# Performance work log

Measured on AMD Instinct MI355X. Metric: run time of the kernel, lower is better.

Reference implementation:

```python
import jax, jax.numpy as jnp
import numpy as np

B, IN_UNITS, IN_CHANNELS, NUM_UNITS, UNIT_SIZE = 128, 32, 4096, 10, 16
NUM_ITER = 3


def setup_inputs() -> dict:
    key = jax.random.key(0)
    k1, k2 = jax.random.split(key)
    # x: primary-capsule output [B, in_units, in_channels]
    x = jax.random.normal(k1, (B, IN_UNITS, IN_CHANNELS), dtype=jnp.float32)
    # W: routing weights, torch param shape [1, C, J, D, K] with batch dim dropped
    W = jax.random.normal(k2, (IN_CHANNELS, NUM_UNITS, UNIT_SIZE, IN_UNITS), dtype=jnp.float32)
    return {"x": x, "W": W}


def reference(x, W):
    b_sz = x.shape[0]
    C, J = W.shape[0], W.shape[1]
    # torch: x.transpose(1,2) -> [B,C,K]; u_hat = W @ x -> [B,C,J,D,1]
    # u_hat[b,i,j,d] = sum_k W[i,j,d,k] * x[b,k,i]
    u_hat = jnp.einsum('ijdk,bki->bijd', W, x)  # [B, C, J, D]
    b_ij = jnp.zeros((C, J), dtype=x.dtype)
    v = None
    for _ in range(NUM_ITER):
        # faithful: softmax over dim=1 (in_channels axis), not over classes
        c_ij = jax.nn.softmax(b_ij, axis=0)               # [C, J]
        s = jnp.einsum('ij,bijd->bjd', c_ij, u_hat)        # [B, J, D]
        # faithful squash: original sums over dim=2 of [B,1,J,D,1] == class axis J
        mag_sq = jnp.sum(s * s, axis=1, keepdims=True)     # [B, 1, D]
        v = (mag_sq / (1.0 + mag_sq)) * (s / jnp.sqrt(mag_sq))
        # agreement: <u_hat, v> averaged over batch
        agree = jnp.einsum('bijd,bjd->ij', u_hat, v) / b_sz
        b_ij = b_ij + agree
    # torch returns v_j.squeeze(1): [B, J, D, 1]
    return v[:, :, :, None]
```

## Files before the change

kernel.cpp:

```cpp
#include <hip/hip_runtime.h>


typedef __attribute__((ext_vector_type(8))) __bf16 bf16x8;
typedef __attribute__((ext_vector_type(4))) float  f32x4;
typedef __attribute__((ext_vector_type(8))) unsigned short u16x8;
typedef __attribute__((ext_vector_type(4))) unsigned short u16x4;

#define DI __device__ __forceinline__

DI float bf2f(unsigned short u){ unsigned int x = ((unsigned int)u) << 16; return __builtin_bit_cast(float, x); }
DI unsigned short f2bf(float f){
  unsigned int u = __builtin_bit_cast(unsigned int, f);
  u += 0x7fffu + ((u >> 16) & 1u);
  return (unsigned short)(u >> 16);
}

constexpr int Ci = 4096, Kk = 32, Jj = 10, Dd = 16, Bb = 128;
constexpr int KI = Ci * Kk;
constexpr int JDt = Jj * Dd;
constexpr int NCH = 256, CK = 512;

constexpr size_t OFF_XB = 0;
constexpr size_t SZ_XB  = (size_t)Bb * KI * 2;
constexpr size_t OFF_W2 = OFF_XB + SZ_XB;
constexpr size_t SZ_W2  = (size_t)JDt * KI * 2;
constexpr size_t OFF_BT = OFF_W2 + SZ_W2;
constexpr size_t SZ_BT  = (size_t)Jj * Ci * 4;
constexpr size_t OFF_CT = OFF_BT + SZ_BT;
constexpr size_t OFF_VBT = OFF_CT + SZ_BT;
constexpr size_t SZ_VBT = (size_t)JDt * Bb * 2;
constexpr size_t OFF_SP = OFF_VBT + SZ_VBT;
constexpr size_t SZ_SP  = (size_t)NCH * Bb * JDt * 4;

__global__ __launch_bounds__(256) void pack_x(const float* __restrict__ x, unsigned short* __restrict__ xbf){
  const size_t e = (size_t)blockIdx.x * 256 + threadIdx.x;
  const float4* xv = (const float4*)x;
  float4 a = xv[e*2], b = xv[e*2+1];
  u16x8 o;
  o[0]=f2bf(a.x); o[1]=f2bf(a.y); o[2]=f2bf(a.z); o[3]=f2bf(a.w);
  o[4]=f2bf(b.x); o[5]=f2bf(b.y); o[6]=f2bf(b.z); o[7]=f2bf(b.w);
  *(u16x8*)(xbf + e*8) = o;
}

__global__ __launch_bounds__(256) void pack_w2(const float* __restrict__ W, unsigned short* __restrict__ w2){
  __shared__ float tile[64][65];
  const int mt = blockIdx.x % 80, it = blockIdx.x / 80;
  const int m0 = mt * 64, i0 = it * 64;
  #pragma unroll
  for(int u=0; u<4; u++){
    int e = threadIdx.x + 256*u;
    int il = e >> 4, q = e & 15;
    float4 v = *(const float4*)(W + (size_t)(i0+il)*5120 + m0 + q*4);
    tile[il][q*4+0]=v.x; tile[il][q*4+1]=v.y; tile[il][q*4+2]=v.z; tile[il][q*4+3]=v.w;
  }
  __syncthreads();
  #pragma unroll
  for(int u=0; u<4; u++){
    int e = threadIdx.x + 256*u;
    int ml = e >> 4, q = e & 15;
    u16x4 o;
    o[0]=f2bf(tile[q*4+0][ml]); o[1]=f2bf(tile[q*4+1][ml]);
    o[2]=f2bf(tile[q*4+2][ml]); o[3]=f2bf(tile[q*4+3][ml]);
    *(u16x4*)(w2 + (size_t)(m0+ml)*Ci + i0 + q*4) = o;
  }
}

__global__ __launch_bounds__(256) void softmax_k(const float* __restrict__ bT, float* __restrict__ cT){
  const int j = blockIdx.x, tid = threadIdx.x, lane = tid & 63, wid = tid >> 6;
  __shared__ float red[4];
  float vals[16];
  float mx = -3.4e38f;
  #pragma unroll
  for(int u=0; u<16; u++){ vals[u] = bT[j*Ci + tid + 256*u]; mx = fmaxf(mx, vals[u]); }
  #pragma unroll
  for(int o=32; o>0; o>>=1) mx = fmaxf(mx, __shfl_xor(mx, o));
  if(lane == 0) red[wid] = mx;
  __syncthreads();
  mx = fmaxf(fmaxf(red[0],red[1]), fmaxf(red[2],red[3]));
  float sm = 0.f;
  #pragma unroll
  for(int u=0; u<16; u++){ vals[u] = expf(vals[u]-mx); sm += vals[u]; }
  #pragma unroll
  for(int o=32; o>0; o>>=1) sm += __shfl_xor(sm, o);
  __syncthreads();
  if(lane == 0) red[wid] = sm;
  __syncthreads();
  sm = red[0]+red[1]+red[2]+red[3];
  float inv = 1.0f / sm;
  #pragma unroll
  for(int u=0; u<16; u++) cT[j*Ci + tid + 256*u] = vals[u]*inv;
}

__global__ __launch_bounds__(512) void s_pass(const unsigned short* __restrict__ xb,
                                              const unsigned short* __restrict__ w2,
                                              const float* __restrict__ cT,
                                              float* __restrict__ spart){
  __shared__ unsigned short xs[128*64];
  __shared__ unsigned short wsm[160*64];
  const int tid = threadIdx.x, lane = tid & 63, wid = tid >> 6;
  const int wb = wid & 3, wj = wid >> 2;
  const int ki0 = blockIdx.x * CK;
  f32x4 acc[2][5];
  const f32x4 z = {0.f,0.f,0.f,0.f};
  #pragma unroll
  for(int m=0;m<2;m++){ acc[m][0]=z; acc[m][1]=z; acc[m][2]=z; acc[m][3]=z; acc[m][4]=z; }

  for(int step=0; step<CK/64; ++step){
    const int kb = ki0 + step*64;
    const int ib = kb & (Ci-1);
    #pragma unroll
    for(int u=0; u<2; u++){
      int e = tid + 512*u;
      int b = e >> 3, sg = e & 7;
      u16x8 v = *(const u16x8*)(xb + (size_t)b*KI + kb + sg*8);
      *(u16x8*)((char*)xs + b*128 + ((sg*16) ^ ((b&7)<<4))) = v;
    }
    #pragma unroll
    for(int u=0; u<3; u++){
      int e = tid + 512*u;
      if(e < 1280){
        int jd = e >> 3, sg = e & 7;
        u16x8 v = *(const u16x8*)(w2 + (size_t)jd*KI + kb + sg*8);
        const float* cp = cT + (jd>>4)*Ci + ib + sg*8;
        float4 c0 = *(const float4*)cp;
        float4 c1 = *(const float4*)(cp+4);
        u16x8 o;
        o[0]=f2bf(bf2f(v[0])*c0.x); o[1]=f2bf(bf2f(v[1])*c0.y);
        o[2]=f2bf(bf2f(v[2])*c0.z); o[3]=f2bf(bf2f(v[3])*c0.w);
        o[4]=f2bf(bf2f(v[4])*c1.x); o[5]=f2bf(bf2f(v[5])*c1.y);
        o[6]=f2bf(bf2f(v[6])*c1.z); o[7]=f2bf(bf2f(v[7])*c1.w);
        *(u16x8*)((char*)wsm + jd*128 + ((sg*16) ^ ((jd&7)<<4))) = o;
      }
    }
    __syncthreads();
    #pragma unroll
    for(int ks=0; ks<2; ks++){
      const int kk2 = (ks*32 + ((lane>>4)<<3)) * 2;
      bf16x8 a[2];
      #pragma unroll
      for(int m=0;m<2;m++){
        int row = wb*32 + m*16 + (lane&15);
        a[m] = *(const bf16x8*)((const char*)xs + row*128 + (kk2 ^ ((row&7)<<4)));
      }
      #pragma unroll
      for(int n=0;n<5;n++){
        int row = wj*80 + n*16 + (lane&15);
        bf16x8 bb = *(const bf16x8*)((const char*)wsm + row*128 + (kk2 ^ ((row&7)<<4)));
        acc[0][n] = __builtin_amdgcn_mfma_f32_16x16x32_bf16(a[0], bb, acc[0][n], 0,0,0);
        acc[1][n] = __builtin_amdgcn_mfma_f32_16x16x32_bf16(a[1], bb, acc[1][n], 0,0,0);
      }
    }
    __syncthreads();
  }
  float* sp = spart + (size_t)blockIdx.x * (Bb*JDt);
  #pragma unroll
  for(int m=0;m<2;m++)
    #pragma unroll
    for(int n=0;n<5;n++)
      #pragma unroll
      for(int r=0;r<4;r++){
        int b  = wb*32 + m*16 + ((lane>>4)<<2) + r;
        int jd = wj*80 + n*16 + (lane&15);
        sp[b*JDt + jd] = acc[m][n][r];
      }
}

__global__ __launch_bounds__(256) void redsq(const float* __restrict__ spart,
                                             float* __restrict__ vout,
                                             unsigned short* __restrict__ vbT){
  const int b = blockIdx.x, tid = threadIdx.x;
  __shared__ float sq[JDt];
  __shared__ float scale[Dd];
  float s = 0.f;
  if(tid < JDt){
    const float* p = spart + b*JDt + tid;
    #pragma unroll 8
    for(int ch=0; ch<NCH; ch++) s += p[(size_t)ch*(Bb*JDt)];
    sq[tid] = s*s;
  }
  __syncthreads();
  if(tid < Dd){
    float m = 0.f;
    #pragma unroll
    for(int j=0;j<Jj;j++) m += sq[j*Dd + tid];
    scale[tid] = sqrtf(m) / (1.0f + m);
  }
  __syncthreads();
  if(tid < JDt){
    float v = s * scale[tid & (Dd-1)];
    vout[b*JDt + tid] = v;
    vbT[tid*Bb + b] = f2bf(v);
  }
}

__global__ __launch_bounds__(256) void agree_pass(const unsigned short* __restrict__ xb,
                                                  const unsigned short* __restrict__ vbT,
                                                  const unsigned short* __restrict__ w2,
                                                  float* __restrict__ bT){
  __shared__ unsigned short xsT[64*128];
  __shared__ unsigned short vsm[160*128];
  const int tid = threadIdx.x, lane = tid & 63, wid = tid >> 6;
  const int wj = wid & 1, wk = wid >> 1;
  const int ki0 = blockIdx.x * 64;
  #pragma unroll
  for(int u=0; u<4; u++){
    int e = tid + 256*u;
    int b = e >> 3, sg = e & 7;
    u16x8 v = *(const u16x8*)(xb + (size_t)b*KI + ki0 + sg*8);
    #pragma unroll
    for(int q=0; q<8; q++){
      int kil = sg*8 + q;
      *(unsigned short*)((char*)xsT + kil*256 + ((b*2) ^ ((kil&7)<<4))) = v[q];
    }
  }
  #pragma unroll
  for(int u=0; u<10; u++){
    int e = tid + 256*u;
    int jd = e >> 4, sg = e & 15;
    u16x8 v = *(const u16x8*)(vbT + jd*Bb + sg*8);
    *(u16x8*)((char*)vsm + jd*256 + ((sg*16) ^ ((jd&7)<<4))) = v;
  }
  __syncthreads();
  f32x4 acc[5][2];
  const f32x4 z = {0.f,0.f,0.f,0.f};
  #pragma unroll
  for(int m=0;m<5;m++){ acc[m][0]=z; acc[m][1]=z; }
  #pragma unroll
  for(int ks=0; ks<4; ks++){
    const int b2 = (ks*32 + ((lane>>4)<<3)) * 2;
    bf16x8 bfr[2];
    #pragma unroll
    for(int n=0;n<2;n++){
      int row = wk*32 + n*16 + (lane&15);
      bfr[n] = *(const bf16x8*)((const char*)xsT + row*256 + (b2 ^ ((row&7)<<4)));
    }
    #pragma unroll
    for(int m=0;m<5;m++){
      int row = wj*80 + m*16 + (lane&15);
      bf16x8 af = *(const bf16x8*)((const char*)vsm + row*256 + (b2 ^ ((row&7)<<4)));
      acc[m][0] = __builtin_amdgcn_mfma_f32_16x16x32_bf16(af, bfr[0], acc[m][0], 0,0,0);
      acc[m][1] = __builtin_amdgcn_mfma_f32_16x16x32_bf16(af, bfr[1], acc[m][1], 0,0,0);
    }
  }
  const int ibase = ki0 & (Ci-1);
  #pragma unroll
  for(int m=0;m<5;m++){
    int j = wj*5 + m;
    #pragma unroll
    for(int n=0;n<2;n++){
      int colg = ki0 + wk*32 + n*16 + (lane&15);
      float s = 0.f;
      #pragma unroll
      for(int r=0;r<4;r++){
        int jdrow = wj*80 + m*16 + ((lane>>4)<<2) + r;
        s += acc[m][n][r] * bf2f(w2[(size_t)jdrow*KI + colg]);
      }
      s += __shfl_xor(s, 16);
      s += __shfl_xor(s, 32);
      if(lane < 16){
        int ig = ibase + wk*32 + n*16 + lane;
        atomicAdd(bT + j*Ci + ig, s * (1.0f/128.0f));
      }
    }
  }
}

extern "C" void kernel_launch(void* const* d_in, const int* in_sizes, int n_in,
                              void* d_out, int out_size, void* d_ws, size_t ws_size,
                              hipStream_t stream) {
  const float* x = (const float*)d_in[0];
  const float* W = (const float*)d_in[1];
  float* out = (float*)d_out;
  char* ws = (char*)d_ws;
  unsigned short* xbf = (unsigned short*)(ws + OFF_XB);
  unsigned short* w2  = (unsigned short*)(ws + OFF_W2);
  float* bT           = (float*)(ws + OFF_BT);
  float* cT           = (float*)(ws + OFF_CT);
  unsigned short* vbT = (unsigned short*)(ws + OFF_VBT);
  float* spart        = (float*)(ws + OFF_SP);

  hipMemsetAsync(bT, 0, SZ_BT, stream);
  pack_x<<<8192, 256, 0, stream>>>(x, xbf);
  pack_w2<<<5120, 256, 0, stream>>>(W, w2);
  for(int t=0; t<3; t++){
    softmax_k<<<Jj, 256, 0, stream>>>(bT, cT);
    s_pass<<<NCH, 512, 0, stream>>>(xbf, w2, cT, spart);
    redsq<<<Bb, 256, 0, stream>>>(spart, out, vbT);
    if(t < 2) agree_pass<<<KI/64, 256, 0, stream>>>(xbf, vbT, w2, bT);
  }
}
```

Before: 236.6 us.

## Double-buffer s_pass, pre-transpose x for agree_pass, skip first softmax, vectorize reductions

s_pass now reads fp32 x directly and converts it in-register with packed bf16 conversion instructions, and double-buffers its LDS tiles so global loads for the next step overlap the MFMAs of the current one. x is pre-transposed into a [KI,B] bf16 layout so agree_pass can load MFMA fragments straight from global memory without LDS staging. The first iteration skips softmax and uses the uniform constant 1/4096, the bT memset is folded into the pack kernel, and redsq splits the channel reduction across more threads with vector loads. This trades extra fp32 x traffic in every s_pass call and uncached global fragment loads for fewer launches and less LDS and sync work.

```diff
diff --git a/kernel.cpp b/kernel.cpp
--- a/kernel.cpp
+++ b/kernel.cpp
@@ -4,7 +4,7 @@
 typedef __attribute__((ext_vector_type(8))) __bf16 bf16x8;
 typedef __attribute__((ext_vector_type(4))) float  f32x4;
 typedef __attribute__((ext_vector_type(8))) unsigned short u16x8;
-typedef __attribute__((ext_vector_type(4))) unsigned short u16x4;
+typedef __attribute__((ext_vector_type(4))) unsigned int  u32x4;
 
 #define DI __device__ __forceinline__
 
@@ -14,17 +14,22 @@
   u += 0x7fffu + ((u >> 16) & 1u);
   return (unsigned short)(u >> 16);
 }
+DI unsigned int cvtpk(float lo, float hi){
+  unsigned int r;
+  asm("v_cvt_pk_bf16_f32 %0, %1, %2" : "=v"(r) : "v"(lo), "v"(hi));
+  return r;
+}
 
 constexpr int Ci = 4096, Kk = 32, Jj = 10, Dd = 16, Bb = 128;
 constexpr int KI = Ci * Kk;
 constexpr int JDt = Jj * Dd;
 constexpr int NCH = 256, CK = 512;
 
-constexpr size_t OFF_XB = 0;
-constexpr size_t SZ_XB  = (size_t)Bb * KI * 2;
-constexpr size_t OFF_W2 = OFF_XB + SZ_XB;
+constexpr size_t OFF_W2 = 0;
 constexpr size_t SZ_W2  = (size_t)JDt * KI * 2;
-constexpr size_t OFF_BT = OFF_W2 + SZ_W2;
+constexpr size_t OFF_XT = OFF_W2 + SZ_W2;
+constexpr size_t SZ_XT  = (size_t)KI * Bb * 2;
+constexpr size_t OFF_BT = OFF_XT + SZ_XT;
 constexpr size_t SZ_BT  = (size_t)Jj * Ci * 4;
 constexpr size_t OFF_CT = OFF_BT + SZ_BT;
 constexpr size_t OFF_VBT = OFF_CT + SZ_BT;
@@ -32,22 +37,12 @@
 constexpr size_t OFF_SP = OFF_VBT + SZ_VBT;
 constexpr size_t SZ_SP  = (size_t)NCH * Bb * JDt * 4;
 
-__global__ __launch_bounds__(256) void pack_x(const float* __restrict__ x, unsigned short* __restrict__ xbf){
-  const size_t e = (size_t)blockIdx.x * 256 + threadIdx.x;
-  const float4* xv = (const float4*)x;
-  float4 a = xv[e*2], b = xv[e*2+1];
-  u16x8 o;
-  o[0]=f2bf(a.x); o[1]=f2bf(a.y); o[2]=f2bf(a.z); o[3]=f2bf(a.w);
-  o[4]=f2bf(b.x); o[5]=f2bf(b.y); o[6]=f2bf(b.z); o[7]=f2bf(b.w);
-  *(u16x8*)(xbf + e*8) = o;
-}
-
-__global__ __launch_bounds__(256) void pack_w2(const float* __restrict__ W, unsigned short* __restrict__ w2){
-  __shared__ float tile[64][65];
+__global__ __launch_bounds__(256) void pack_w(const float* __restrict__ W, unsigned short* __restrict__ w2){
+  __shared__ float tile[128][65];
   const int mt = blockIdx.x % 80, it = blockIdx.x / 80;
-  const int m0 = mt * 64, i0 = it * 64;
-  #pragma unroll
-  for(int u=0; u<4; u++){
+  const int m0 = mt * 64, i0 = it * 128;
+  #pragma unroll
+  for(int u=0; u<8; u++){
     int e = threadIdx.x + 256*u;
     int il = e >> 4, q = e & 15;
     float4 v = *(const float4*)(W + (size_t)(i0+il)*5120 + m0 + q*4);
@@ -58,10 +53,42 @@
   for(int u=0; u<4; u++){
     int e = threadIdx.x + 256*u;
     int ml = e >> 4, q = e & 15;
-    u16x4 o;
-    o[0]=f2bf(tile[q*4+0][ml]); o[1]=f2bf(tile[q*4+1][ml]);
-    o[2]=f2bf(tile[q*4+2][ml]); o[3]=f2bf(tile[q*4+3][ml]);
-    *(u16x4*)(w2 + (size_t)(m0+ml)*Ci + i0 + q*4) = o;
+    u32x4 o;
+    o[0]=cvtpk(tile[q*8+0][ml], tile[q*8+1][ml]);
+    o[1]=cvtpk(tile[q*8+2][ml], tile[q*8+3][ml]);
+    o[2]=cvtpk(tile[q*8+4][ml], tile[q*8+5][ml]);
+    o[3]=cvtpk(tile[q*8+6][ml], tile[q*8+7][ml]);
+    *(u32x4*)(w2 + (size_t)(m0+ml)*Ci + i0 + q*8) = o;
+  }
+}
+
+__global__ __launch_bounds__(256) void pack_xt(const float* __restrict__ x, unsigned short* __restrict__ xT,
+                                               float* __restrict__ bT){
+  __shared__ float tile[128][65];
+  const int bid = blockIdx.x;
+  if(bid >= 2048){
+    ((f32x4*)bT)[(bid-2048)*256 + threadIdx.x] = f32x4{0.f,0.f,0.f,0.f};
+    return;
+  }
+  const int ki0 = bid * 64;
+  #pragma unroll
+  for(int u=0; u<8; u++){
+    int e = threadIdx.x + 256*u;
+    int bl = e >> 4, q = e & 15;
+    float4 v = *(const float4*)(x + (size_t)bl*KI + ki0 + q*4);
+    tile[bl][q*4+0]=v.x; tile[bl][q*4+1]=v.y; tile[bl][q*4+2]=v.z; tile[bl][q*4+3]=v.w;
+  }
+  __syncthreads();
+  #pragma unroll
+  for(int u=0; u<4; u++){
+    int e = threadIdx.x + 256*u;
+    int kil = e >> 4, g = e & 15;
+    u32x4 o;
+    o[0]=cvtpk(tile[g*8+0][kil], tile[g*8+1][kil]);
+    o[1]=cvtpk(tile[g*8+2][kil], tile[g*8+3][kil]);
+    o[2]=cvtpk(tile[g*8+4][kil], tile[g*8+5][kil]);
+    o[3]=cvtpk(tile[g*8+6][kil], tile[g*8+7][kil]);
+    *(u32x4*)(xT + (size_t)(ki0+kil)*Bb + g*8) = o;
   }
 }
 
@@ -91,48 +118,73 @@
   for(int u=0; u<16; u++) cT[j*Ci + tid + 256*u] = vals[u]*inv;
 }
 
-__global__ __launch_bounds__(512) void s_pass(const unsigned short* __restrict__ xb,
+__global__ __launch_bounds__(512) void s_pass(const float* __restrict__ x,
                                               const unsigned short* __restrict__ w2,
                                               const float* __restrict__ cT,
                                               float* __restrict__ spart){
-  __shared__ unsigned short xs[128*64];
-  __shared__ unsigned short wsm[160*64];
+  __shared__ unsigned short xs[2][128*64];
+  __shared__ unsigned short wsm[2][160*64];
   const int tid = threadIdx.x, lane = tid & 63, wid = tid >> 6;
   const int wb = wid & 3, wj = wid >> 2;
   const int ki0 = blockIdx.x * CK;
+  const float cu = 1.0f/4096.0f;
+
+  const int xb_ = tid >> 3, xsg = tid & 7;
   f32x4 acc[2][5];
-  const f32x4 z = {0.f,0.f,0.f,0.f};
-  #pragma unroll
-  for(int m=0;m<2;m++){ acc[m][0]=z; acc[m][1]=z; acc[m][2]=z; acc[m][3]=z; acc[m][4]=z; }
-
-  for(int step=0; step<CK/64; ++step){
-    const int kb = ki0 + step*64;
-    const int ib = kb & (Ci-1);
-    #pragma unroll
-    for(int u=0; u<2; u++){
-      int e = tid + 512*u;
-      int b = e >> 3, sg = e & 7;
-      u16x8 v = *(const u16x8*)(xb + (size_t)b*KI + kb + sg*8);
-      *(u16x8*)((char*)xs + b*128 + ((sg*16) ^ ((b&7)<<4))) = v;
-    }
-    #pragma unroll
-    for(int u=0; u<3; u++){
-      int e = tid + 512*u;
-      if(e < 1280){
-        int jd = e >> 3, sg = e & 7;
-        u16x8 v = *(const u16x8*)(w2 + (size_t)jd*KI + kb + sg*8);
-        const float* cp = cT + (jd>>4)*Ci + ib + sg*8;
-        float4 c0 = *(const float4*)cp;
-        float4 c1 = *(const float4*)(cp+4);
-        u16x8 o;
-        o[0]=f2bf(bf2f(v[0])*c0.x); o[1]=f2bf(bf2f(v[1])*c0.y);
-        o[2]=f2bf(bf2f(v[2])*c0.z); o[3]=f2bf(bf2f(v[3])*c0.w);
-        o[4]=f2bf(bf2f(v[4])*c1.x); o[5]=f2bf(bf2f(v[5])*c1.y);
-        o[6]=f2bf(bf2f(v[6])*c1.z); o[7]=f2bf(bf2f(v[7])*c1.w);
-        *(u16x8*)((char*)wsm + jd*128 + ((sg*16) ^ ((jd&7)<<4))) = o;
-      }
-    }
-    __syncthreads();
+  #pragma unroll
+  for(int m=0;m<2;m++)
+    #pragma unroll
+    for(int n=0;n<5;n++) acc[m][n] = f32x4{0.f,0.f,0.f,0.f};
+
+  float4 xv[4]; u16x8 wv[3]; float4 cv[3][2];
+
+  #define S_LOAD(STEP) { \
+    const int kb = ki0 + (STEP)*64; \
+    const float* xr = x + (size_t)xb_*KI + kb + xsg*8; \
+    xv[0]=*(const float4*)xr; xv[1]=*(const float4*)(xr+4); \
+    const float* xr2 = xr + (size_t)64*KI; \
+    xv[2]=*(const float4*)xr2; xv[3]=*(const float4*)(xr2+4); \
+    const int ib = kb & (Ci-1); \
+    _Pragma("unroll") \
+    for(int u=0; u<3; u++){ int e = tid + 512*u; if(e < 1280){ \
+      int jd = e>>3, sg = e&7; \
+      wv[u] = *(const u16x8*)(w2 + (size_t)jd*KI + kb + sg*8); \
+      if(cT){ const float* cp = cT + (jd>>4)*Ci + ib + sg*8; \
+        cv[u][0] = *(const float4*)cp; cv[u][1] = *(const float4*)(cp+4); } \
+    }} }
+
+  #define S_WRITE(BUF) { \
+    u32x4 xo; \
+    xo[0]=cvtpk(xv[0].x,xv[0].y); xo[1]=cvtpk(xv[0].z,xv[0].w); \
+    xo[2]=cvtpk(xv[1].x,xv[1].y); xo[3]=cvtpk(xv[1].z,xv[1].w); \
+    *(u32x4*)((char*)xs[BUF] + xb_*128 + ((xsg*16) ^ ((xb_&7)<<4))) = xo; \
+    xo[0]=cvtpk(xv[2].x,xv[2].y); xo[1]=cvtpk(xv[2].z,xv[2].w); \
+    xo[2]=cvtpk(xv[3].x,xv[3].y); xo[3]=cvtpk(xv[3].z,xv[3].w); \
+    *(u32x4*)((char*)xs[BUF] + (xb_+64)*128 + ((xsg*16) ^ ((xb_&7)<<4))) = xo; \
+    _Pragma("unroll") \
+    for(int u=0; u<3; u++){ int e = tid + 512*u; if(e < 1280){ \
+      int jd = e>>3, sg = e&7; \
+      float f[8]; \
+      _Pragma("unroll") \
+      for(int q=0;q<8;q++) f[q] = bf2f(wv[u][q]); \
+      if(cT){ \
+        f[0]*=cv[u][0].x; f[1]*=cv[u][0].y; f[2]*=cv[u][0].z; f[3]*=cv[u][0].w; \
+        f[4]*=cv[u][1].x; f[5]*=cv[u][1].y; f[6]*=cv[u][1].z; f[7]*=cv[u][1].w; \
+      } else { \
+        _Pragma("unroll") \
+        for(int q=0;q<8;q++) f[q] *= cu; \
+      } \
+      u32x4 wo; \
+      wo[0]=cvtpk(f[0],f[1]); wo[1]=cvtpk(f[2],f[3]); \
+      wo[2]=cvtpk(f[4],f[5]); wo[3]=cvtpk(f[6],f[7]); \
+      *(u32x4*)((char*)wsm[BUF] + jd*128 + ((sg*16) ^ ((jd&7)<<4))) = wo; \
+    }} }
+
+  S_LOAD(0); S_WRITE(0);
+  __syncthreads();
+  int cur = 0;
+  for(int step=0; step<8; ++step){
+    if(step < 7) S_LOAD(step+1);
     #pragma unroll
     for(int ks=0; ks<2; ks++){
       const int kk2 = (ks*32 + ((lane>>4)<<3)) * 2;
@@ -140,17 +192,19 @@
       #pragma unroll
       for(int m=0;m<2;m++){
         int row = wb*32 + m*16 + (lane&15);
-        a[m] = *(const bf16x8*)((const char*)xs + row*128 + (kk2 ^ ((row&7)<<4)));
+        a[m] = *(const bf16x8*)((const char*)xs[cur] + row*128 + (kk2 ^ ((row&7)<<4)));
       }
       #pragma unroll
       for(int n=0;n<5;n++){
         int row = wj*80 + n*16 + (lane&15);
-        bf16x8 bb = *(const bf16x8*)((const char*)wsm + row*128 + (kk2 ^ ((row&7)<<4)));
+        bf16x8 bb = *(const bf16x8*)((const char*)wsm[cur] + row*128 + (kk2 ^ ((row&7)<<4)));
         acc[0][n] = __builtin_amdgcn_mfma_f32_16x16x32_bf16(a[0], bb, acc[0][n], 0,0,0);
         acc[1][n] = __builtin_amdgcn_mfma_f32_16x16x32_bf16(a[1], bb, acc[1][n], 0,0,0);
       }
     }
+    if(step < 7) S_WRITE(cur^1);
     __syncthreads();
+    cur ^= 1;
   }
   float* sp = spart + (size_t)blockIdx.x * (Bb*JDt);
   #pragma unroll
@@ -169,13 +223,21 @@
                                              float* __restrict__ vout,
                                              unsigned short* __restrict__ vbT){
   const int b = blockIdx.x, tid = threadIdx.x;
+  __shared__ float sred[6][JDt];
   __shared__ float sq[JDt];
   __shared__ float scale[Dd];
+  if(tid < 240){
+    const int g = tid % 40, cg = tid / 40;
+    f32x4 a = {0.f,0.f,0.f,0.f};
+    for(int ch=cg; ch<NCH; ch+=6)
+      a += *(const f32x4*)(spart + (size_t)ch*(Bb*JDt) + b*JDt + g*4);
+    *(f32x4*)&sred[cg][g*4] = a;
+  }
+  __syncthreads();
   float s = 0.f;
   if(tid < JDt){
-    const float* p = spart + b*JDt + tid;
-    #pragma unroll 8
-    for(int ch=0; ch<NCH; ch++) s += p[(size_t)ch*(Bb*JDt)];
+    #pragma unroll
+    for(int c=0;c<6;c++) s += sred[c][tid];
     sq[tid] = s*s;
   }
   __syncthreads();
@@ -193,53 +255,32 @@
   }
 }
 
-__global__ __launch_bounds__(256) void agree_pass(const unsigned short* __restrict__ xb,
+__global__ __launch_bounds__(256) void agree_pass(const unsigned short* __restrict__ xT,
                                                   const unsigned short* __restrict__ vbT,
                                                   const unsigned short* __restrict__ w2,
                                                   float* __restrict__ bT){
-  __shared__ unsigned short xsT[64*128];
-  __shared__ unsigned short vsm[160*128];
   const int tid = threadIdx.x, lane = tid & 63, wid = tid >> 6;
   const int wj = wid & 1, wk = wid >> 1;
   const int ki0 = blockIdx.x * 64;
-  #pragma unroll
-  for(int u=0; u<4; u++){
-    int e = tid + 256*u;
-    int b = e >> 3, sg = e & 7;
-    u16x8 v = *(const u16x8*)(xb + (size_t)b*KI + ki0 + sg*8);
-    #pragma unroll
-    for(int q=0; q<8; q++){
-      int kil = sg*8 + q;
-      *(unsigned short*)((char*)xsT + kil*256 + ((b*2) ^ ((kil&7)<<4))) = v[q];
+  const int bsl = (lane>>4)<<3;
+  f32x4 acc[5][2];
+  #pragma unroll
+  for(int m=0;m<5;m++){ acc[m][0]=f32x4{0,0,0,0}; acc[m][1]=f32x4{0,0,0,0}; }
+  #pragma unroll
+  for(int ks=0; ks<4; ks++){
+    bf16x8 af[5];
+    #pragma unroll
+    for(int m=0;m<5;m++){
+      int jd = wj*80 + m*16 + (lane&15);
+      af[m] = *(const bf16x8*)(vbT + jd*Bb + ks*32 + bsl);
     }
-  }
-  #pragma unroll
-  for(int u=0; u<10; u++){
-    int e = tid + 256*u;
-    int jd = e >> 4, sg = e & 15;
-    u16x8 v = *(const u16x8*)(vbT + jd*Bb + sg*8);
-    *(u16x8*)((char*)vsm + jd*256 + ((sg*16) ^ ((jd&7)<<4))) = v;
-  }
-  __syncthreads();
-  f32x4 acc[5][2];
-  const f32x4 z = {0.f,0.f,0.f,0.f};
-  #pragma unroll
-  for(int m=0;m<5;m++){ acc[m][0]=z; acc[m][1]=z; }
-  #pragma unroll
-  for(int ks=0; ks<4; ks++){
-    const int b2 = (ks*32 + ((lane>>4)<<3)) * 2;
-    bf16x8 bfr[2];
     #pragma unroll
     for(int n=0;n<2;n++){
-      int row = wk*32 + n*16 + (lane&15);
-      bfr[n] = *(const bf16x8*)((const char*)xsT + row*256 + (b2 ^ ((row&7)<<4)));
-    }
-    #pragma unroll
-    for(int m=0;m<5;m++){
-      int row = wj*80 + m*16 + (lane&15);
-      bf16x8 af = *(const bf16x8*)((const char*)vsm + row*256 + (b2 ^ ((row&7)<<4)));
-      acc[m][0] = __builtin_amdgcn_mfma_f32_16x16x32_bf16(af, bfr[0], acc[m][0], 0,0,0);
-      acc[m][1] = __builtin_amdgcn_mfma_f32_16x16x32_bf16(af, bfr[1], acc[m][1], 0,0,0);
+      int kir = ki0 + wk*32 + n*16 + (lane&15);
+      bf16x8 bf_ = *(const bf16x8*)(xT + (size_t)kir*Bb + ks*32 + bsl);
+      #pragma unroll
+      for(int m=0;m<5;m++)
+        acc[m][n] = __builtin_amdgcn_mfma_f32_16x16x32_bf16(af[m], bf_, acc[m][n], 0,0,0);
     }
   }
   const int ibase = ki0 & (Ci-1);
@@ -272,20 +313,19 @@
   const float* W = (const float*)d_in[1];
   float* out = (float*)d_out;
   char* ws = (char*)d_ws;
-  unsigned short* xbf = (unsigned short*)(ws + OFF_XB);
   unsigned short* w2  = (unsigned short*)(ws + OFF_W2);
+  unsigned short* xT  = (unsigned short*)(ws + OFF_XT);
   float* bT           = (float*)(ws + OFF_BT);
   float* cT           = (float*)(ws + OFF_CT);
   unsigned short* vbT = (unsigned short*)(ws + OFF_VBT);
   float* spart        = (float*)(ws + OFF_SP);
 
-  hipMemsetAsync(bT, 0, SZ_BT, stream);
-  pack_x<<<8192, 256, 0, stream>>>(x, xbf);
-  pack_w2<<<5120, 256, 0, stream>>>(W, w2);
+  pack_w<<<2560, 256, 0, stream>>>(W, w2);
+  pack_xt<<<2088, 256, 0, stream>>>(x, xT, bT);
   for(int t=0; t<3; t++){
-    softmax_k<<<Jj, 256, 0, stream>>>(bT, cT);
-    s_pass<<<NCH, 512, 0, stream>>>(xbf, w2, cT, spart);
+    if(t > 0) softmax_k<<<Jj, 256, 0, stream>>>(bT, cT);
+    s_pass<<<NCH, 512, 0, stream>>>(x, w2, (t==0)? nullptr : cT, spart);
     redsq<<<Bb, 256, 0, stream>>>(spart, out, vbT);
-    if(t < 2) agree_pass<<<KI/64, 256, 0, stream>>>(xbf, vbT, w2, bT);
-  }
-}
+    if(t < 2) agree_pass<<<KI/64, 256, 0, stream>>>(xT, vbT, w2, bT);
+  }
+}
```

Measured after the change: 234.3 us. About the same (-1.0%).
